# Kernel tuning notes

Measured on AMD Instinct MI355X. Metric: run time of the kernel, lower is better.

The kernel has to match this reference:

```python
import jax, jax.numpy as jnp
import numpy as np

B = 65536
N_WORKER, N_PROJECT, EMB = 1807, 2490, 10
STATE_DIM = 2 * EMB          # 20
HIDDEN = 2 * STATE_DIM       # 40
ACTION_DIM = EMB             # 10


def setup_inputs() -> dict:
    key = jax.random.key(0)
    ks = jax.random.split(key, 8)
    worker_ids = jax.random.randint(ks[0], (B,), 0, N_WORKER)
    project_ids = jax.random.randint(ks[1], (B,), 0, N_PROJECT)
    worker_emb = jax.random.normal(ks[2], (N_WORKER, EMB), dtype=jnp.float32)
    project_emb = jax.random.normal(ks[3], (N_PROJECT, EMB), dtype=jnp.float32)
    W1 = jax.random.normal(ks[4], (HIDDEN, STATE_DIM), dtype=jnp.float32) / np.sqrt(STATE_DIM)
    b1 = jnp.zeros((HIDDEN,), dtype=jnp.float32)
    W2 = jax.random.normal(ks[5], (ACTION_DIM, HIDDEN), dtype=jnp.float32) / np.sqrt(HIDDEN)
    b2 = jnp.zeros((ACTION_DIM,), dtype=jnp.float32)
    return {"worker_ids": worker_ids, "project_ids": project_ids,
            "worker_emb": worker_emb, "project_emb": project_emb,
            "W1": W1, "b1": b1, "W2": W2, "b2": b2}


def reference(worker_ids, project_ids, worker_emb, project_emb, W1, b1, W2, b2):
    we = worker_emb[worker_ids]              # [B, 10]
    pe = project_emb[project_ids]            # [B, 10]
    x = jnp.concatenate([we, pe], axis=-1)   # [B, 20]
    h = jax.nn.relu(x @ W1.T + b1)           # [B, 40]
    the_weights = (h @ W2.T + b2)[:, None, :]  # [B, 1, 10]
    # original loop rebuilds rows 1..2489 of the project table -> single slice
    table = project_emb[1:N_PROJECT]         # [2489, 10]
    p = jnp.einsum('bqd,nd->bqn', the_weights, table)  # [B, 1, 2489]
    argmax = jnp.argmax(p, axis=2)           # [B, 1]
    return argmax + 1
```

## Files before the change

### kernel.cpp

```cpp
#include <hip/hip_runtime.h>
#include <float.h>

using v2f = __attribute__((ext_vector_type(2))) float;
using v4f = __attribute__((ext_vector_type(4))) float;

#define EMB 10
#define STATE 20
#define HIDDEN 40
#define NPROJ 2490

__device__ __forceinline__ void score_pair(const v4f* __restrict__ tbl4, int p,
                                           const v2f wv2[5],
                                           float& best, int& bidx) {
    const v4f* tp = tbl4 + p * 5;
    v4f a0 = tp[0], a1 = tp[1], a2 = tp[2], a3 = tp[3], a4 = tp[4];
    v2f c0 = wv2[0] * a0.lo;
    c0 += wv2[1] * a0.hi; c0 += wv2[2] * a1.lo;
    c0 += wv2[3] * a1.hi; c0 += wv2[4] * a2.lo;
    float s0 = c0.x + c0.y;
    v2f c1 = wv2[0] * a2.hi;
    c1 += wv2[1] * a3.lo; c1 += wv2[2] * a3.hi;
    c1 += wv2[3] * a4.lo; c1 += wv2[4] * a4.hi;
    float s1 = c1.x + c1.y;
    float sp = s0; int ip = 2 * p;
    if (s1 > sp) { sp = s1; ip = 2 * p + 1; }
    if (sp > best) { best = sp; bidx = ip; }
}

__global__ __launch_bounds__(256, 2) void actor_kernel(
    const int* __restrict__ wid, const int* __restrict__ pid,
    const float* __restrict__ wemb, const float* __restrict__ pemb,
    const float* __restrict__ W1, const float* __restrict__ b1,
    const float* __restrict__ W2, const float* __restrict__ b2,
    int* __restrict__ out)
{
    __shared__ float sb[4][64];
    __shared__ int   si[4][64];

    const int tid  = threadIdx.x;
    const int lane = tid & 63;
    const int wave = tid >> 6;
    const int g    = wave >> 1;
    const int h    = wave & 1;
    const int b    = blockIdx.x * 128 + g * 64 + lane;

    const v4f* __restrict__ tbl4 =
        (const v4f*)__builtin_assume_aligned(pemb, 16);

    const int wi = wid[b];
    const int pi = pid[b];
    const float* __restrict__ wr = wemb + wi * EMB;
    const float* __restrict__ pr = pemb + pi * EMB;
    v2f x2[STATE / 2];
    #pragma unroll
    for (int k = 0; k < EMB / 2; ++k) x2[k] = *(const v2f*)(wr + 2 * k);
    #pragma unroll
    for (int k = 0; k < EMB / 2; ++k) x2[EMB / 2 + k] = *(const v2f*)(pr + 2 * k);

    float hb[HIDDEN];
    #pragma unroll 4
    for (int j = 0; j < HIDDEN; ++j) {
        const v2f* w1r = (const v2f*)(W1 + j * STATE);
        v2f a = w1r[0] * x2[0];
        #pragma unroll
        for (int k = 1; k < STATE / 2; ++k) a += w1r[k] * x2[k];
        hb[j] = fmaxf(a.x + a.y + b1[j], 0.0f);
    }
    v2f h2[HIDDEN / 2];
    #pragma unroll
    for (int k = 0; k < HIDDEN / 2; ++k) h2[k] = (v2f){hb[2 * k], hb[2 * k + 1]};

    v2f wv2[5];
    #pragma unroll
    for (int d = 0; d < EMB; d += 2) {
        const v2f* w2r0 = (const v2f*)(W2 + d * HIDDEN);
        const v2f* w2r1 = (const v2f*)(W2 + (d + 1) * HIDDEN);
        v2f a0 = w2r0[0] * h2[0];
        v2f a1 = w2r1[0] * h2[0];
        #pragma unroll
        for (int k = 1; k < HIDDEN / 2; ++k) { a0 += w2r0[k] * h2[k]; a1 += w2r1[k] * h2[k]; }
        wv2[d / 2] = (v2f){a0.x + a0.y + b2[d], a1.x + a1.y + b2[d + 1]};
    }

    float best = -FLT_MAX;
    int   bidx = 1;

    if (h == 0) {
        {
            v2f c0v = *(const v2f*)(pemb + 10);
            v4f c1v = *(const v4f*)(pemb + 12);
            v4f c2v = *(const v4f*)(pemb + 16);
            v2f a = wv2[0] * c0v;
            a += wv2[1] * c1v.lo; a += wv2[2] * c1v.hi;
            a += wv2[3] * c2v.lo; a += wv2[4] * c2v.hi;
            best = a.x + a.y; bidx = 1;
        }
        #pragma unroll 4
        for (int p = 1; p < 623; ++p) score_pair(tbl4, p, wv2, best, bidx);
    } else {
        #pragma unroll 4
        for (int p = 623; p < 1245; ++p) score_pair(tbl4, p, wv2, best, bidx);
    }

    sb[wave][lane] = best;
    si[wave][lane] = bidx;
    __syncthreads();
    if (h == 0) {
        float v  = sb[wave + 1][lane];
        int   vi = si[wave + 1][lane];
        if (v > best) { best = v; bidx = vi; }
        out[b] = bidx;
    }
}

extern "C" void kernel_launch(void* const* d_in, const int* in_sizes, int n_in,
                              void* d_out, int out_size, void* d_ws, size_t ws_size,
                              hipStream_t stream) {
    const int*   wid  = (const int*)  d_in[0];
    const int*   pid  = (const int*)  d_in[1];
    const float* wemb = (const float*)d_in[2];
    const float* pemb = (const float*)d_in[3];
    const float* W1   = (const float*)d_in[4];
    const float* b1   = (const float*)d_in[5];
    const float* W2   = (const float*)d_in[6];
    const float* b2   = (const float*)d_in[7];
    int* out = (int*)d_out;

    const int B = in_sizes[0];
    actor_kernel<<<B / 128, 256, 0, stream>>>(wid, pid, wemb, pemb, W1, b1, W2, b2, out);
}
```

Baseline: 137.3 us.

## Split candidate scan across eight waves and compute MLP once per row

Each block now handles 64 batch rows with 8 waves. One wave computes the MLP and shares the 10-element weight vector through shared memory, and all 8 waves each scan about an eighth of the project table before wave 0 reduces the partial argmaxes. This removes the duplicated MLP work of the previous two-wave split and spreads the scoring loop more finely. The cost is idle waves during the MLP phase, an extra barrier, and tighter register limits from the launch bounds.

```diff
diff --git a/kernel.cpp b/kernel.cpp
--- a/kernel.cpp
+++ b/kernel.cpp
@@ -27,88 +27,97 @@
     if (sp > best) { best = sp; bidx = ip; }
 }
 
-__global__ __launch_bounds__(256, 2) void actor_kernel(
+__global__ __launch_bounds__(512, 8) void actor_kernel(
     const int* __restrict__ wid, const int* __restrict__ pid,
     const float* __restrict__ wemb, const float* __restrict__ pemb,
     const float* __restrict__ W1, const float* __restrict__ b1,
     const float* __restrict__ W2, const float* __restrict__ b2,
     int* __restrict__ out)
 {
-    __shared__ float sb[4][64];
-    __shared__ int   si[4][64];
+    __shared__ v2f   sw[64][5];
+    __shared__ float sb[8][64];
+    __shared__ int   si[8][64];
 
     const int tid  = threadIdx.x;
     const int lane = tid & 63;
     const int wave = tid >> 6;
-    const int g    = wave >> 1;
-    const int h    = wave & 1;
-    const int b    = blockIdx.x * 128 + g * 64 + lane;
+    const int b    = blockIdx.x * 64 + lane;
 
     const v4f* __restrict__ tbl4 =
         (const v4f*)__builtin_assume_aligned(pemb, 16);
 
-    const int wi = wid[b];
-    const int pi = pid[b];
-    const float* __restrict__ wr = wemb + wi * EMB;
-    const float* __restrict__ pr = pemb + pi * EMB;
-    v2f x2[STATE / 2];
-    #pragma unroll
-    for (int k = 0; k < EMB / 2; ++k) x2[k] = *(const v2f*)(wr + 2 * k);
-    #pragma unroll
-    for (int k = 0; k < EMB / 2; ++k) x2[EMB / 2 + k] = *(const v2f*)(pr + 2 * k);
+    if (wave == 0) {
+        const int wi = wid[b];
+        const int pi = pid[b];
+        const float* __restrict__ wr = wemb + wi * EMB;
+        const float* __restrict__ pr = pemb + pi * EMB;
+        v2f x2[STATE / 2];
+        #pragma unroll
+        for (int k = 0; k < EMB / 2; ++k) x2[k] = *(const v2f*)(wr + 2 * k);
+        #pragma unroll
+        for (int k = 0; k < EMB / 2; ++k) x2[EMB / 2 + k] = *(const v2f*)(pr + 2 * k);
 
-    float hb[HIDDEN];
-    #pragma unroll 4
-    for (int j = 0; j < HIDDEN; ++j) {
-        const v2f* w1r = (const v2f*)(W1 + j * STATE);
-        v2f a = w1r[0] * x2[0];
+        float hb[HIDDEN];
+        #pragma unroll 4
+        for (int j = 0; j < HIDDEN; ++j) {
+            const v2f* w1r = (const v2f*)(W1 + j * STATE);
+            v2f a = w1r[0] * x2[0];
+            #pragma unroll
+            for (int k = 1; k < STATE / 2; ++k) a += w1r[k] * x2[k];
+            hb[j] = fmaxf(a.x + a.y + b1[j], 0.0f);
+        }
+        v2f h2[HIDDEN / 2];
         #pragma unroll
-        for (int k = 1; k < STATE / 2; ++k) a += w1r[k] * x2[k];
-        hb[j] = fmaxf(a.x + a.y + b1[j], 0.0f);
+        for (int k = 0; k < HIDDEN / 2; ++k) h2[k] = (v2f){hb[2 * k], hb[2 * k + 1]};
+
+        #pragma unroll
+        for (int d = 0; d < EMB; d += 2) {
+            const v2f* w2r0 = (const v2f*)(W2 + d * HIDDEN);
+            const v2f* w2r1 = (const v2f*)(W2 + (d + 1) * HIDDEN);
+            v2f a0 = w2r0[0] * h2[0];
+            v2f a1 = w2r1[0] * h2[0];
+            #pragma unroll
+            for (int k = 1; k < HIDDEN / 2; ++k) { a0 += w2r0[k] * h2[k]; a1 += w2r1[k] * h2[k]; }
+            sw[lane][d / 2] = (v2f){a0.x + a0.y + b2[d], a1.x + a1.y + b2[d + 1]};
+        }
     }
-    v2f h2[HIDDEN / 2];
-    #pragma unroll
-    for (int k = 0; k < HIDDEN / 2; ++k) h2[k] = (v2f){hb[2 * k], hb[2 * k + 1]};
+    __syncthreads();
 
     v2f wv2[5];
     #pragma unroll
-    for (int d = 0; d < EMB; d += 2) {
-        const v2f* w2r0 = (const v2f*)(W2 + d * HIDDEN);
-        const v2f* w2r1 = (const v2f*)(W2 + (d + 1) * HIDDEN);
-        v2f a0 = w2r0[0] * h2[0];
-        v2f a1 = w2r1[0] * h2[0];
-        #pragma unroll
-        for (int k = 1; k < HIDDEN / 2; ++k) { a0 += w2r0[k] * h2[k]; a1 += w2r1[k] * h2[k]; }
-        wv2[d / 2] = (v2f){a0.x + a0.y + b2[d], a1.x + a1.y + b2[d + 1]};
+    for (int k = 0; k < 5; ++k) wv2[k] = sw[lane][k];
+
+    float best = -FLT_MAX;
+    int   bidx = 0;
+
+    const int extra = (wave < 4) ? wave : 4;
+    const int start = 1 + wave * 155 + extra;
+    const int end   = start + 155 + ((wave < 4) ? 1 : 0);
+
+    if (wave == 0) {
+        v2f c0v = *(const v2f*)(pemb + 10);
+        v4f c1v = *(const v4f*)(pemb + 12);
+        v4f c2v = *(const v4f*)(pemb + 16);
+        v2f a = wv2[0] * c0v;
+        a += wv2[1] * c1v.lo; a += wv2[2] * c1v.hi;
+        a += wv2[3] * c2v.lo; a += wv2[4] * c2v.hi;
+        best = a.x + a.y; bidx = 1;
     }
 
-    float best = -FLT_MAX;
-    int   bidx = 1;
-
-    if (h == 0) {
-        {
-            v2f c0v = *(const v2f*)(pemb + 10);
-            v4f c1v = *(const v4f*)(pemb + 12);
-            v4f c2v = *(const v4f*)(pemb + 16);
-            v2f a = wv2[0] * c0v;
-            a += wv2[1] * c1v.lo; a += wv2[2] * c1v.hi;
-            a += wv2[3] * c2v.lo; a += wv2[4] * c2v.hi;
-            best = a.x + a.y; bidx = 1;
-        }
-        #pragma unroll 4
-        for (int p = 1; p < 623; ++p) score_pair(tbl4, p, wv2, best, bidx);
-    } else {
-        #pragma unroll 4
-        for (int p = 623; p < 1245; ++p) score_pair(tbl4, p, wv2, best, bidx);
-    }
+    #pragma unroll 4
+    for (int p = start; p < end; ++p) score_pair(tbl4, p, wv2, best, bidx);
 
     sb[wave][lane] = best;
     si[wave][lane] = bidx;
     __syncthreads();
-    if (h == 0) {
-        float v  = sb[wave + 1][lane];
-        int   vi = si[wave + 1][lane];
-        if (v > best) { best = v; bidx = vi; }
+
+    if (wave == 0) {
+        #pragma unroll
+        for (int w = 1; w < 8; ++w) {
+            float v  = sb[w][lane];
+            int   vi = si[w][lane];
+            if (v > best) { best = v; bidx = vi; }
+        }
         out[b] = bidx;
     }
 }
@@ -127,5 +136,5 @@
     int* out = (int*)d_out;
 
     const int B = in_sizes[0];
-    actor_kernel<<<B / 128, 256, 0, stream>>>(wid, pid, wemb, pemb, W1, b1, W2, b2, out);
+    actor_kernel<<<B / 64, 512, 0, stream>>>(wid, pid, wemb, pemb, W1, b1, W2, b2, out);
 }
```

Measured after the change: 255.2 us. +85.9%, slower.
